# Optimization experiments

Hardware: AMD Instinct MI355X
Metric: run time of the kernel (lower is better)

The kernel has to match this reference:

```python
import jax, jax.numpy as jnp
import numpy as np
from jax import lax

V, E, H = 10000, 512, 512
B, L, T = 128, 8, 48


def setup_inputs() -> dict:
    key = jax.random.key(0)
    ks = jax.random.split(key, 12)
    s = lambda k, shape: jax.random.normal(k, shape, jnp.float32) * 0.05
    kw_lens = jnp.sort(jax.random.randint(ks[2], (B,), 1, L + 1))[::-1]  # descending, as pack_padded requires
    return {
        "kws": jax.random.randint(ks[0], (B, L), 0, V),
        "poem": jax.random.randint(ks[1], (B, T), 0, V),
        "kw_lens": kw_lens,
        "embedding": s(ks[3], (V, E)),
        "enc_Wih": s(ks[4], (4 * H, E)), "enc_Whh": s(ks[5], (4 * H, H)), "enc_b": s(ks[6], (4 * H,)),
        "dec_Wih": s(ks[7], (4 * H, E)), "dec_Whh": s(ks[8], (4 * H, H)), "dec_b": s(ks[9], (4 * H,)),
        "out_W": s(ks[10], (V, 2 * H)), "out_b": s(ks[11], (V,)),
    }


def _lstm_step(h, c, x, Wih, Whh, b):
    # PyTorch gate order: i, f, g, o
    gates = x @ Wih.T + h @ Whh.T + b  # [B, 4H]
    i, f, g, o = jnp.split(gates, 4, axis=-1)
    c = jax.nn.sigmoid(f) * c + jax.nn.sigmoid(i) * jnp.tanh(g)
    h = jax.nn.sigmoid(o) * jnp.tanh(c)
    return h, c


def reference(kws, poem, kw_lens, embedding, enc_Wih, enc_Whh, enc_b,
              dec_Wih, dec_Whh, dec_b, out_W, out_b):
    bs = kws.shape[0]
    mask = jnp.arange(L)[None, :] < kw_lens[:, None]  # sequence_mask, [B, L]

    # ---- encoder LSTM over keywords (dropout inactive at eval) ----
    kws_emb = embedding[kws]  # [B, L, E]

    def enc_scan(carry, x):
        h, c = carry
        h, c = _lstm_step(h, c, x, enc_Wih, enc_Whh, enc_b)
        return (h, c), (h, c)

    z = jnp.zeros((bs, H), embedding.dtype)
    _, (hs, cs) = lax.scan(enc_scan, (z, z), kws_emb.transpose(1, 0, 2))  # [L, B, H]
    kws_rep = hs.transpose(1, 0, 2) * mask[..., None]  # pad_packed zeros past length
    # pack semantics: final hidden is the state at the last valid timestep
    bidx = jnp.arange(bs)
    h0 = hs[kw_lens - 1, bidx]
    c0 = cs[kw_lens - 1, bidx]

    # ---- greedy per-timestep decode with dot-product attention ----
    neg = jnp.asarray(-1e9, embedding.dtype)

    def dec_scan(carry, tok):
        h, c = carry
        x = embedding[tok]  # [B, E]
        h, c = _lstm_step(h, c, x, dec_Wih, dec_Whh, dec_b)
        scores = jnp.einsum('bh,blh->bl', h, kws_rep)
        attn = jax.nn.softmax(jnp.where(mask, scores, neg), axis=-1)
        ctx = jnp.einsum('bl,blh->bh', attn, kws_rep)
        logits = jnp.concatenate([h, ctx], axis=-1) @ out_W.T + out_b  # [B, V]
        return (h, c), logits

    _, preds = lax.scan(dec_scan, (h0, c0), poem.T)  # [T, B, V]
    return preds.transpose(1, 0, 2)  # [B, T, V]
```

## Files before the change

kernel.cpp:

```cpp
#include <hip/hip_runtime.h>
#include <hip/hip_bf16.h>

typedef __bf16 bf16;
typedef __attribute__((ext_vector_type(8))) __bf16 bf16x8;
typedef __attribute__((ext_vector_type(4))) __bf16 bf16x4;
typedef __attribute__((ext_vector_type(4))) float f32x4;

#define B_ 128
#define L_ 8
#define T_ 48
#define V_ 10000
#define NBLK_REC 32

__device__ __forceinline__ float sigf(float x) { return 1.f / (1.f + expf(-x)); }

__device__ __forceinline__ void gl_lds16(const bf16* g, bf16* l) {
  __builtin_amdgcn_global_load_lds(
      (const __attribute__((address_space(1))) unsigned int*)g,
      (__attribute__((address_space(3))) unsigned int*)l, 16, 0, 0);
}

__device__ __forceinline__ unsigned aload32(const void* p) {
  return __hip_atomic_load((unsigned*)p, __ATOMIC_RELAXED, __HIP_MEMORY_SCOPE_AGENT);
}
__device__ __forceinline__ void astore64(void* p, unsigned long long v) {
  __hip_atomic_store((unsigned long long*)p, v, __ATOMIC_RELAXED, __HIP_MEMORY_SCOPE_AGENT);
}
__device__ __forceinline__ float bflo(unsigned u) { return __uint_as_float(u << 16); }
__device__ __forceinline__ float bfhi(unsigned u) { return __uint_as_float(u & 0xffff0000u); }
__device__ __forceinline__ unsigned packbf(float lo, float hi) {
  bf16 a = (bf16)lo, b = (bf16)hi;
  unsigned short ua = __builtin_bit_cast(unsigned short, a);
  unsigned short ub = __builtin_bit_cast(unsigned short, b);
  return (unsigned)ua | ((unsigned)ub << 16);
}

__device__ __forceinline__ void signal(unsigned* flg, int blk, unsigned step) {
  asm volatile("s_waitcnt vmcnt(0)" ::: "memory");
  __syncthreads();
  if (threadIdx.x == 0)
    __hip_atomic_store(flg + blk * 32, step, __ATOMIC_RELAXED, __HIP_MEMORY_SCOPE_AGENT);
}
__device__ __forceinline__ void waitstep(const unsigned* flg, unsigned step) {
  if (threadIdx.x < 64) {
    int lane = threadIdx.x;
    for (;;) {
      unsigned v = (lane < NBLK_REC) ? aload32(flg + lane * 32) : step;
      if (__all((int)(v >= step))) break;
      __builtin_amdgcn_s_sleep(1);
    }
  }
  __syncthreads();
}

__global__ void prep_kernel(
    const int* __restrict__ kws, const int* __restrict__ poem,
    const float* __restrict__ emb,
    const float* __restrict__ eWih, const float* __restrict__ eWhh,
    const float* __restrict__ dWih, const float* __restrict__ dWhh,
    const float* __restrict__ outW,
    bf16* __restrict__ WihE, bf16* __restrict__ WhhE,
    bf16* __restrict__ WihD, bf16* __restrict__ WhhD,
    bf16* __restrict__ outWb,
    bf16* __restrict__ Xenc, bf16* __restrict__ Xdec,
    unsigned* __restrict__ flg)
{
  if (blockIdx.x == 0)
    for (int i = threadIdx.x; i < 1024; i += blockDim.x) flg[i] = 0u;
  const long SW = 1048576;
  const long SOWP = 10354688;
  const long SXE = 524288;
  const long SXD = 3145728;
  const long total = 4 * SW + SOWP + SXE + SXD;
  for (long i = blockIdx.x * (long)blockDim.x + threadIdx.x; i < total;
       i += (long)gridDim.x * blockDim.x) {
    long j = i;
    if (j < SW) { WihE[j] = (bf16)eWih[j]; continue; } j -= SW;
    if (j < SW) { WhhE[j] = (bf16)eWhh[j]; continue; } j -= SW;
    if (j < SW) { WihD[j] = (bf16)dWih[j]; continue; } j -= SW;
    if (j < SW) { WhhD[j] = (bf16)dWhh[j]; continue; } j -= SW;
    if (j < SOWP) {
      long r = j >> 10;
      outWb[j] = (r < 10000) ? (bf16)outW[j] : (bf16)0.f;
      continue;
    } j -= SOWP;
    if (j < SXE) {
      int e = (int)(j & 511); int b = (int)((j >> 9) & 127); int l = (int)(j >> 16);
      int tok = kws[b * L_ + l];
      Xenc[j] = (bf16)emb[(long)tok * 512 + e];
      continue;
    } j -= SXE;
    {
      int e = (int)(j & 511); int b = (int)((j >> 9) & 127); int t = (int)(j >> 16);
      int tok = poem[b * T_ + t];
      Xdec[j] = (bf16)emb[(long)tok * 512 + e];
    }
  }
}

template<int MODE>
__global__ __launch_bounds__(256) void gemm2_kernel(
    const bf16* __restrict__ A, const bf16* __restrict__ Bm,
    const float* __restrict__ bias, void* __restrict__ outp,
    int M, int N, int K, int MT)
{
  __shared__ bf16 As[128 * 32];
  __shared__ bf16 Bs[128 * 32];
  const int tid = threadIdx.x, lane = tid & 63, wid = tid >> 6;
  const int nwg = gridDim.x;
  int bid = blockIdx.x;
  int tm, tn;
  if (MODE == 2) {
    int xcd = bid & 7, idx = bid >> 3;
    tm = xcd * 6 + idx % 6;
    tn = idx / 6;
  } else {
    int swz = ((nwg & 7) == 0) ? ((bid & 7) * (nwg >> 3) + (bid >> 3)) : bid;
    tm = swz % MT; tn = swz / MT;
  }
  const int m0 = tm * 128, n0 = tn * 128;
  const int wm = (wid >> 1) * 64, wn = (wid & 1) * 64;
  const int fr = lane & 15, ku = lane >> 4;

  f32x4 acc[4][4];
  #pragma unroll
  for (int mi = 0; mi < 4; ++mi)
    #pragma unroll
    for (int ni = 0; ni < 4; ++ni) {
      acc[mi][ni][0] = 0.f; acc[mi][ni][1] = 0.f;
      acc[mi][ni][2] = 0.f; acc[mi][ni][3] = 0.f;
    }

  for (int kt = 0; kt < K; kt += 32) {
    #pragma unroll
    for (int j = 0; j < 2; ++j) {
      int i0 = j * 256 + wid * 64;
      int i = i0 + lane;
      int r = i >> 2, ub = i & 3;
      gl_lds16(A + (size_t)(m0 + r) * K + kt + ub * 8, As + (size_t)i0 * 8);
      gl_lds16(Bm + (size_t)(n0 + r) * K + kt + ub * 8, Bs + (size_t)i0 * 8);
    }
    __syncthreads();
    bf16x8 af[4], bfr[4];
    #pragma unroll
    for (int mi = 0; mi < 4; ++mi)
      af[mi] = *(const bf16x8*)(As + (size_t)(wm + mi * 16 + fr) * 32 + ku * 8);
    #pragma unroll
    for (int ni = 0; ni < 4; ++ni)
      bfr[ni] = *(const bf16x8*)(Bs + (size_t)(wn + ni * 16 + fr) * 32 + ku * 8);
    #pragma unroll
    for (int mi = 0; mi < 4; ++mi)
      #pragma unroll
      for (int ni = 0; ni < 4; ++ni)
        acc[mi][ni] = __builtin_amdgcn_mfma_f32_16x16x32_bf16(af[mi], bfr[ni], acc[mi][ni], 0, 0, 0);
    __syncthreads();
  }

  const int fq = (lane >> 4) * 4;
  #pragma unroll
  for (int mi = 0; mi < 4; ++mi) {
    #pragma unroll
    for (int ni = 0; ni < 4; ++ni) {
      #pragma unroll
      for (int j = 0; j < 4; ++j) {
        int r = m0 + wm + mi * 16 + fq + j;
        int cix = n0 + wn + ni * 16 + fr;
        if (cix < N) {
          float v = acc[mi][ni][j] + bias[cix];
          if (MODE == 2) {
            int b = r & 127, t = r >> 7;
            ((float*)outp)[(size_t)b * (T_ * V_) + (size_t)t * V_ + cix] = v;
          } else {
            ((bf16*)outp)[((size_t)(r >> 7) * 2048 + cix) * 128 + (r & 127)] = (bf16)v;
          }
        }
      }
    }
  }
}

__global__ __launch_bounds__(256, 1) void recurrent_kernel(
    const bf16* __restrict__ preEncT, const bf16* __restrict__ preDecT,
    const bf16* __restrict__ WhhE, const bf16* __restrict__ WhhD,
    const int* __restrict__ kwl,
    bf16* __restrict__ hS,
    bf16* __restrict__ h0b,
    bf16* __restrict__ hsEnc,
    bf16* __restrict__ Hcat,
    unsigned* __restrict__ flg)
{
  __shared__ bf16 Bs[64 * 512];
  __shared__ bf16 As[128 * 256];
  const int tid = threadIdx.x, lane = tid & 63, wid = tid >> 6;
  const int blk = blockIdx.x, n0 = blk * 16;
  const int fr = lane & 15, fq = (lane >> 4) * 4, ku = lane >> 4;
  const int axor = fr & 7;
  const int arow0 = wid * 32 + fr, arow1 = wid * 32 + 16 + fr;
  const int row0 = wid * 32 + fq, row1 = wid * 32 + 16 + fq;
  const int brow = tid >> 1, bhalf = tid & 1;
  const int blen = kwl[brow];
  const int batt = blk * 4 + wid;
  const int lenb = kwl[batt];
  int lenr[2][4];
  #pragma unroll
  for (int j = 0; j < 4; ++j) { lenr[0][j] = kwl[row0 + j]; lenr[1][j] = kwl[row1 + j]; }

  auto loadB = [&](const bf16* W) {
    #pragma unroll
    for (int j = 0; j < 16; ++j) {
      int i = j * 256 + tid;
      int r = i >> 6, u = i & 63;
      int p = u ^ (r & 7);
      bf16x8 v = *(const bf16x8*)(W + (size_t)((r >> 4) * 512 + n0 + (r & 15)) * 512 + u * 8);
      *(bf16x8*)(Bs + (size_t)r * 512 + p * 8) = v;
    }
  };

  f32x4 acc[2][4];
  auto zacc = [&]() {
    #pragma unroll
    for (int mi = 0; mi < 2; ++mi)
      #pragma unroll
      for (int g = 0; g < 4; ++g) {
        acc[mi][g][0] = 0.f; acc[mi][g][1] = 0.f;
        acc[mi][g][2] = 0.f; acc[mi][g][3] = 0.f;
      }
  };

  auto gemm_full = [&](const bf16* h_in) {
    #pragma unroll
    for (int ch = 0; ch < 2; ++ch) {
      f32x4 tv[16];
      #pragma unroll
      for (int j = 0; j < 16; ++j) {
        int i = j * 256 + tid;
        int r = i >> 5, up = i & 31;
        const bf16* ga = h_in + (size_t)r * 512 + ch * 256 + up * 8;
        asm volatile("global_load_dwordx4 %0, %1, off sc0 sc1"
                     : "=v"(tv[j]) : "v"(ga) : "memory");
      }
      asm volatile("s_waitcnt vmcnt(0)" ::: "memory");
      __builtin_amdgcn_sched_barrier(0);
      #pragma unroll
      for (int j = 0; j < 16; ++j) {
        int i = j * 256 + tid;
        int r = i >> 5, up = i & 31;
        int s = up ^ (r & 7);
        *(f32x4*)(As + ((size_t)r * 32 + s) * 8) = tv[j];
      }
      __syncthreads();
      #pragma unroll
      for (int kt = 0; kt < 8; ++kt) {
        int cA = (kt * 4 + ku) ^ axor;
        int cB = ((ch * 8 + kt) * 4 + ku) ^ axor;
        bf16x8 af0 = *(const bf16x8*)(As + (size_t)arow0 * 256 + cA * 8);
        bf16x8 af1 = *(const bf16x8*)(As + (size_t)arow1 * 256 + cA * 8);
        #pragma unroll
        for (int g = 0; g < 4; ++g) {
          bf16x8 bv = *(const bf16x8*)(Bs + (size_t)(g * 16 + fr) * 512 + cB * 8);
          acc[0][g] = __builtin_amdgcn_mfma_f32_16x16x32_bf16(af0, bv, acc[0][g], 0, 0, 0);
          acc[1][g] = __builtin_amdgcn_mfma_f32_16x16x32_bf16(af1, bv, acc[1][g], 0, 0, 0);
        }
      }
      __syncthreads();
    }
  };

  float cr[2][4] = {{0.f,0.f,0.f,0.f},{0.f,0.f,0.f,0.f}};
  float c0r[2][4] = {{0.f,0.f,0.f,0.f},{0.f,0.f,0.f,0.f}};
  bf16 hout[2][4];

  bf16x4 gv[2][4];
  auto prefg = [&](const bf16* preT) {
    #pragma unroll
    for (int mi = 0; mi < 2; ++mi) {
      int rbase = mi ? row1 : row0;
      int hcol = n0 + fr;
      #pragma unroll
      for (int g = 0; g < 4; ++g)
        gv[mi][g] = *(const bf16x4*)(preT + ((size_t)(g * 512 + hcol)) * 128 + rbase);
    }
  };

  auto pointwise = [&]() {
    #pragma unroll
    for (int mi = 0; mi < 2; ++mi) {
      #pragma unroll
      for (int j = 0; j < 4; ++j) {
        float gi = acc[mi][0][j] + (float)gv[mi][0][j];
        float gf = acc[mi][1][j] + (float)gv[mi][1][j];
        float gg = acc[mi][2][j] + (float)gv[mi][2][j];
        float go = acc[mi][3][j] + (float)gv[mi][3][j];
        float cn = sigf(gf) * cr[mi][j] + sigf(gi) * tanhf(gg);
        float hn = sigf(go) * tanhf(cn);
        cr[mi][j] = cn;
        hout[mi][j] = (bf16)hn;
      }
    }
  };

  auto bounce_store = [&](bf16* hdst, bf16* hsdst, int t, int is_enc) {
    #pragma unroll
    for (int mi = 0; mi < 2; ++mi) {
      int rbase = mi ? row1 : row0;
      #pragma unroll
      for (int j = 0; j < 4; ++j)
        As[(size_t)(rbase + j) * 16 + fr] = hout[mi][j];
    }
    __syncthreads();
    unsigned long long v0 = *(unsigned long long*)(As + (size_t)brow * 16 + bhalf * 8);
    unsigned long long v1 = *(unsigned long long*)(As + (size_t)brow * 16 + bhalf * 8 + 4);
    size_t off = (size_t)brow * 512 + n0 + bhalf * 8;
    astore64(hdst + off, v0);
    astore64(hdst + off + 4, v1);
    if (is_enc) {
      unsigned long long m0 = (t < blen) ? v0 : 0ull;
      unsigned long long m1 = (t < blen) ? v1 : 0ull;
      astore64(hsdst + off, m0);
      astore64(hsdst + off + 4, m1);
      if (t == blen - 1) {
        astore64(h0b + off, v0);
        astore64(h0b + off + 4, v1);
      }
    }
  };

  unsigned hatt[4];
  auto load_hatt = [&](const bf16* h_in) {
    #pragma unroll
    for (int e = 0; e < 4; ++e)
      hatt[e] = aload32(h_in + (size_t)batt * 512 + lane * 2 + 128 * e);
  };

  unsigned hsr[8][4];

  auto attention = [&](int tprev) {
    float sc[8];
    #pragma unroll
    for (int l = 0; l < 8; ++l) {
      float p = 0.f;
      #pragma unroll
      for (int e = 0; e < 4; ++e)
        p += bflo(hatt[e]) * bflo(hsr[l][e]) + bfhi(hatt[e]) * bfhi(hsr[l][e]);
      #pragma unroll
      for (int off = 32; off; off >>= 1) p += __shfl_xor(p, off);
      sc[l] = p;
    }
    float m = -1e30f;
    #pragma unroll
    for (int l = 0; l < 8; ++l) m = fmaxf(m, (l < lenb) ? sc[l] : -1e30f);
    float wgt[8]; float den = 0.f;
    #pragma unroll
    for (int l = 0; l < 8; ++l) { wgt[l] = (l < lenb) ? expf(sc[l] - m) : 0.f; den += wgt[l]; }
    float inv = 1.f / den;
    bf16* dst = Hcat + ((size_t)tprev * 128 + batt) * 1024;
    #pragma unroll
    for (int e = 0; e < 4; ++e) {
      float clo = 0.f, chi = 0.f;
      #pragma unroll
      for (int l = 0; l < 8; ++l) {
        clo += wgt[l] * bflo(hsr[l][e]);
        chi += wgt[l] * bfhi(hsr[l][e]);
      }
      *(unsigned*)(dst + 512 + lane * 2 + 128 * e) = packbf(clo * inv, chi * inv);
      *(unsigned*)(dst + lane * 2 + 128 * e) = hatt[e];
    }
  };

  loadB(WhhE);
  __syncthreads();
  for (int t = 0; t < 8; ++t) {
    prefg(preEncT + (size_t)t * 262144);
    zacc();
    if (t > 0) {
      waitstep(flg, (unsigned)t);
      gemm_full(hS + (size_t)(t - 1) * 65536);
    }
    pointwise();
    #pragma unroll
    for (int mi = 0; mi < 2; ++mi)
      #pragma unroll
      for (int j = 0; j < 4; ++j)
        if (t == lenr[mi][j] - 1) c0r[mi][j] = cr[mi][j];
    bounce_store(hS + (size_t)t * 65536, hsEnc + (size_t)t * 65536, t, 1);
    signal(flg, blk, (unsigned)(t + 1));
  }

  __syncthreads();
  loadB(WhhD);
  __syncthreads();
  waitstep(flg, 8u);
  #pragma unroll
  for (int l = 0; l < 8; ++l)
    #pragma unroll
    for (int e = 0; e < 4; ++e)
      hsr[l][e] = aload32(hsEnc + ((size_t)l * 128 + batt) * 512 + lane * 2 + 128 * e);
  #pragma unroll
  for (int mi = 0; mi < 2; ++mi)
    #pragma unroll
    for (int j = 0; j < 4; ++j) cr[mi][j] = c0r[mi][j];

  for (int t = 0; t < 48; ++t) {
    prefg(preDecT + (size_t)t * 262144);
    zacc();
    const bf16* hin = (t == 0) ? (const bf16*)h0b : (const bf16*)(hS + (size_t)(8 + t - 1) * 65536);
    waitstep(flg, (unsigned)(8 + t));
    gemm_full(hin);
    pointwise();
    bounce_store(hS + (size_t)(8 + t) * 65536, nullptr, t, 0);
    signal(flg, blk, (unsigned)(9 + t));
    if (t >= 1) {
      load_hatt(hin);
      attention(t - 1);
    }
  }
  waitstep(flg, 56u);
  load_hatt(hS + (size_t)55 * 65536);
  attention(47);
}

extern "C" void kernel_launch(void* const* d_in, const int* in_sizes, int n_in,
                              void* d_out, int out_size, void* d_ws, size_t ws_size,
                              hipStream_t stream)
{
  const int* kws  = (const int*)d_in[0];
  const int* poem = (const int*)d_in[1];
  const int* kwl  = (const int*)d_in[2];
  const float* emb  = (const float*)d_in[3];
  const float* eWih = (const float*)d_in[4];
  const float* eWhh = (const float*)d_in[5];
  const float* eb   = (const float*)d_in[6];
  const float* dWih = (const float*)d_in[7];
  const float* dWhh = (const float*)d_in[8];
  const float* db   = (const float*)d_in[9];
  const float* outW = (const float*)d_in[10];
  const float* outb = (const float*)d_in[11];
  float* out = (float*)d_out;

  char* base = (char*)d_ws;
  size_t o = 0;
  auto take = [&](size_t bytes) -> char* {
    char* r = base + o;
    o += (bytes + 255) & ~(size_t)255;
    return r;
  };
  bf16* WihE  = (bf16*)take(2048 * 512 * 2);
  bf16* WhhE  = (bf16*)take(2048 * 512 * 2);
  bf16* WihD  = (bf16*)take(2048 * 512 * 2);
  bf16* WhhD  = (bf16*)take(2048 * 512 * 2);
  bf16* outWb = (bf16*)take((size_t)10112 * 1024 * 2);
  bf16* Xenc  = (bf16*)take(1024 * 512 * 2);
  bf16* Xdec  = (bf16*)take((size_t)6144 * 512 * 2);
  bf16* preEncT = (bf16*)take((size_t)8 * 2048 * 128 * 2);
  bf16* preDecT = (bf16*)take((size_t)48 * 2048 * 128 * 2);
  bf16* Hcat   = (bf16*)take((size_t)6144 * 1024 * 2);
  bf16* hS     = (bf16*)take((size_t)56 * 65536 * 2);
  bf16* hsEnc  = (bf16*)take((size_t)8 * 128 * 512 * 2);
  bf16* h0b    = (bf16*)take(128 * 512 * 2);
  unsigned* flg = (unsigned*)take(4096);

  prep_kernel<<<4096, 256, 0, stream>>>(kws, poem, emb, eWih, eWhh, dWih, dWhh, outW,
                                        WihE, WhhE, WihD, WhhD, outWb, Xenc, Xdec, flg);

  gemm2_kernel<3><<<128, 256, 0, stream>>>(Xenc, WihE, eb, preEncT, 1024, 2048, 512, 8);
  gemm2_kernel<3><<<768, 256, 0, stream>>>(Xdec, WihD, db, preDecT, 6144, 2048, 512, 48);

  recurrent_kernel<<<NBLK_REC, 256, 0, stream>>>(preEncT, preDecT, WhhE, WhhD, kwl,
                                                 hS, h0b, hsEnc, Hcat, flg);

  gemm2_kernel<2><<<3792, 256, 0, stream>>>(Hcat, outWb, outb, out, 6144, 10000, 1024, 48);
}
```

Measured before the change: 788.1 us.

## Confine recurrent LSTM to 16 blocks on one XCD with gate-interleaved layout

The recurrent kernel now launches 128 blocks, and each block reads its XCC_ID and claims a role through atomics. Only the first 16 blocks on the first XCD to fill up keep running, so the per-step flag barrier and h exchange stay within one XCD's L2 and can use sc0 loads and stores instead of device-scope coherent traffic. Each block holds a 128x512 slice of Whh in LDS covering all four gates interleaved, and the pre-activation layout is changed to put the gates adjacent, so the pointwise step reads gates locally. Risks include wasted blocks, a timeout-based fallback if the XCD election fails, and a heavier per-block GEMM.

```diff
diff --git a/kernel.cpp b/kernel.cpp
--- a/kernel.cpp
+++ b/kernel.cpp
@@ -10,7 +10,8 @@
 #define L_ 8
 #define T_ 48
 #define V_ 10000
-#define NBLK_REC 32
+#define NB 128
+#define ROLES 16
 
 __device__ __forceinline__ float sigf(float x) { return 1.f / (1.f + expf(-x)); }
 
@@ -19,12 +20,15 @@
       (const __attribute__((address_space(1))) unsigned int*)g,
       (__attribute__((address_space(3))) unsigned int*)l, 16, 0, 0);
 }
-
-__device__ __forceinline__ unsigned aload32(const void* p) {
-  return __hip_atomic_load((unsigned*)p, __ATOMIC_RELAXED, __HIP_MEMORY_SCOPE_AGENT);
-}
-__device__ __forceinline__ void astore64(void* p, unsigned long long v) {
-  __hip_atomic_store((unsigned long long*)p, v, __ATOMIC_RELAXED, __HIP_MEMORY_SCOPE_AGENT);
+__device__ __forceinline__ void gl_lds16_c(const bf16* g, bf16* l) {
+  __builtin_amdgcn_global_load_lds(
+      (const __attribute__((address_space(1))) unsigned int*)g,
+      (__attribute__((address_space(3))) unsigned int*)l, 16, 0, 1);
+}
+
+__device__ __forceinline__ void st2_sc0(bf16* p, unsigned short v) {
+  unsigned v32 = v;
+  asm volatile("global_store_short %0, %1, off sc0" :: "v"(p), "v"(v32) : "memory");
 }
 __device__ __forceinline__ float bflo(unsigned u) { return __uint_as_float(u << 16); }
 __device__ __forceinline__ float bfhi(unsigned u) { return __uint_as_float(u & 0xffff0000u); }
@@ -33,24 +37,6 @@
   unsigned short ua = __builtin_bit_cast(unsigned short, a);
   unsigned short ub = __builtin_bit_cast(unsigned short, b);
   return (unsigned)ua | ((unsigned)ub << 16);
-}
-
-__device__ __forceinline__ void signal(unsigned* flg, int blk, unsigned step) {
-  asm volatile("s_waitcnt vmcnt(0)" ::: "memory");
-  __syncthreads();
-  if (threadIdx.x == 0)
-    __hip_atomic_store(flg + blk * 32, step, __ATOMIC_RELAXED, __HIP_MEMORY_SCOPE_AGENT);
-}
-__device__ __forceinline__ void waitstep(const unsigned* flg, unsigned step) {
-  if (threadIdx.x < 64) {
-    int lane = threadIdx.x;
-    for (;;) {
-      unsigned v = (lane < NBLK_REC) ? aload32(flg + lane * 32) : step;
-      if (__all((int)(v >= step))) break;
-      __builtin_amdgcn_s_sleep(1);
-    }
-  }
-  __syncthreads();
 }
 
 __global__ void prep_kernel(
@@ -63,10 +49,10 @@
     bf16* __restrict__ WihD, bf16* __restrict__ WhhD,
     bf16* __restrict__ outWb,
     bf16* __restrict__ Xenc, bf16* __restrict__ Xdec,
-    unsigned* __restrict__ flg)
+    unsigned* __restrict__ ctl)
 {
   if (blockIdx.x == 0)
-    for (int i = threadIdx.x; i < 1024; i += blockDim.x) flg[i] = 0u;
+    for (int i = threadIdx.x; i < 8192; i += blockDim.x) ctl[i] = 0u;
   const long SW = 1048576;
   const long SOWP = 10354688;
   const long SXE = 524288;
@@ -171,7 +157,9 @@
             int b = r & 127, t = r >> 7;
             ((float*)outp)[(size_t)b * (T_ * V_) + (size_t)t * V_ + cix] = v;
           } else {
-            ((bf16*)outp)[((size_t)(r >> 7) * 2048 + cix) * 128 + (r & 127)] = (bf16)v;
+            int t = r >> 7, b = r & 127;
+            int hcol = cix & 511, g = cix >> 9;
+            ((bf16*)outp)[(((size_t)t * 512 + hcol) * 128 + b) * 4 + g] = (bf16)v;
           }
         }
       }
@@ -183,238 +171,272 @@
     const bf16* __restrict__ preEncT, const bf16* __restrict__ preDecT,
     const bf16* __restrict__ WhhE, const bf16* __restrict__ WhhD,
     const int* __restrict__ kwl,
-    bf16* __restrict__ hS,
-    bf16* __restrict__ h0b,
-    bf16* __restrict__ hsEnc,
-    bf16* __restrict__ Hcat,
-    unsigned* __restrict__ flg)
+    bf16* __restrict__ hS, bf16* __restrict__ h0b,
+    bf16* __restrict__ hsEnc, bf16* __restrict__ Hcat,
+    unsigned* __restrict__ ctl)
 {
-  __shared__ bf16 Bs[64 * 512];
-  __shared__ bf16 As[128 * 256];
+  __shared__ bf16 Wlds[128 * 512];
+  __shared__ bf16 Hb[128 * 128];
+  int* s_info = (int*)Hb;
   const int tid = threadIdx.x, lane = tid & 63, wid = tid >> 6;
-  const int blk = blockIdx.x, n0 = blk * 16;
-  const int fr = lane & 15, fq = (lane >> 4) * 4, ku = lane >> 4;
-  const int axor = fr & 7;
-  const int arow0 = wid * 32 + fr, arow1 = wid * 32 + 16 + fr;
-  const int row0 = wid * 32 + fq, row1 = wid * 32 + 16 + fq;
-  const int brow = tid >> 1, bhalf = tid & 1;
-  const int blen = kwl[brow];
-  const int batt = blk * 4 + wid;
-  const int lenb = kwl[batt];
-  int lenr[2][4];
+
+  if (tid == 0) {
+    unsigned xcd;
+    asm volatile("s_getreg_b32 %0, hwreg(HW_REG_XCC_ID)" : "=s"(xcd));
+    xcd &= 7u;
+    unsigned r = __hip_atomic_fetch_add(ctl + xcd, 1u, __ATOMIC_RELAXED, __HIP_MEMORY_SCOPE_AGENT);
+    asm volatile("s_waitcnt vmcnt(0)" ::: "memory");
+    __hip_atomic_fetch_add(ctl + 8, 1u, __ATOMIC_RELAXED, __HIP_MEMORY_SCOPE_AGENT);
+    int iters = 0;
+    while (__hip_atomic_load(ctl + 8, __ATOMIC_RELAXED, __HIP_MEMORY_SCOPE_AGENT) < NB &&
+           iters++ < (1 << 20))
+      __builtin_amdgcn_s_sleep(8);
+    int win = -1;
+    for (int x = 0; x < 8; ++x) {
+      unsigned c = __hip_atomic_load(ctl + x, __ATOMIC_RELAXED, __HIP_MEMORY_SCOPE_AGENT);
+      if (win < 0 && c >= ROLES) win = x;
+    }
+    s_info[0] = (int)r;
+    s_info[1] = ((int)xcd == win && r < ROLES) ? 1 : 0;
+    s_info[2] = (int)xcd;
+  }
+  __syncthreads();
+  const int role = s_info[0];
+  const int ok = s_info[1];
+  const int myxcd = s_info[2];
+  __syncthreads();
+  if (!ok) return;
+  unsigned* flgx = ctl + 512 + myxcd * (ROLES * 32);
+  unsigned* myflag = flgx + role * 32;
+
+  const int fr = lane & 15, ku = lane >> 4;
+  const int wm2 = wid >> 1, wn2 = wid & 1;
+  const int b0 = (role * 4 + wid) * 2;
+  const int lenb0 = kwl[b0], lenb1 = kwl[b0 + 1];
+  int lenB[4];
   #pragma unroll
-  for (int j = 0; j < 4; ++j) { lenr[0][j] = kwl[row0 + j]; lenr[1][j] = kwl[row1 + j]; }
-
-  auto loadB = [&](const bf16* W) {
-    #pragma unroll
-    for (int j = 0; j < 16; ++j) {
-      int i = j * 256 + tid;
+  for (int ni = 0; ni < 4; ++ni) lenB[ni] = kwl[wn2 * 64 + ni * 16 + fr];
+
+  auto signal = [&](unsigned step) {
+    asm volatile("s_waitcnt vmcnt(0)" ::: "memory");
+    __syncthreads();
+    if (tid == 0)
+      asm volatile("global_store_dword %0, %1, off sc0" :: "v"(myflag), "v"(step) : "memory");
+  };
+  auto waitstep = [&](unsigned step) {
+    if (tid < 64) {
+      const unsigned* fp = flgx + (tid & 15) * 32;
+      const bool act = tid < ROLES;
+      int iters = 0;
+      for (;;) {
+        unsigned v = step;
+        if (act)
+          asm volatile("global_load_dword %0, %1, off sc0\n\ts_waitcnt vmcnt(0)"
+                       : "=v"(v) : "v"(fp) : "memory");
+        if (__all((int)(v >= step)) || iters++ > (1 << 20)) break;
+        __builtin_amdgcn_s_sleep(2);
+      }
+    }
+    __syncthreads();
+  };
+
+  auto loadW = [&](const bf16* W) {
+    #pragma unroll
+    for (int q = 0; q < 32; ++q) {
+      int i = q * 256 + tid;
       int r = i >> 6, u = i & 63;
-      int p = u ^ (r & 7);
-      bf16x8 v = *(const bf16x8*)(W + (size_t)((r >> 4) * 512 + n0 + (r & 15)) * 512 + u * 8);
-      *(bf16x8*)(Bs + (size_t)r * 512 + p * 8) = v;
-    }
-  };
-
-  f32x4 acc[2][4];
+      int j5 = r >> 2, g = r & 3;
+      bf16x8 v = *(const bf16x8*)(W + (size_t)(g * 512 + role * 32 + j5) * 512 + u * 8);
+      *(bf16x8*)(Wlds + ((size_t)r * 64 + (u ^ (r & 15))) * 8) = v;
+    }
+  };
+
+  f32x4 acc[4][4];
   auto zacc = [&]() {
     #pragma unroll
-    for (int mi = 0; mi < 2; ++mi)
-      #pragma unroll
-      for (int g = 0; g < 4; ++g) {
-        acc[mi][g][0] = 0.f; acc[mi][g][1] = 0.f;
-        acc[mi][g][2] = 0.f; acc[mi][g][3] = 0.f;
-      }
-  };
-
-  auto gemm_full = [&](const bf16* h_in) {
-    #pragma unroll
-    for (int ch = 0; ch < 2; ++ch) {
-      f32x4 tv[16];
-      #pragma unroll
-      for (int j = 0; j < 16; ++j) {
-        int i = j * 256 + tid;
-        int r = i >> 5, up = i & 31;
-        const bf16* ga = h_in + (size_t)r * 512 + ch * 256 + up * 8;
-        asm volatile("global_load_dwordx4 %0, %1, off sc0 sc1"
-                     : "=v"(tv[j]) : "v"(ga) : "memory");
-      }
-      asm volatile("s_waitcnt vmcnt(0)" ::: "memory");
-      __builtin_amdgcn_sched_barrier(0);
-      #pragma unroll
-      for (int j = 0; j < 16; ++j) {
-        int i = j * 256 + tid;
-        int r = i >> 5, up = i & 31;
-        int s = up ^ (r & 7);
-        *(f32x4*)(As + ((size_t)r * 32 + s) * 8) = tv[j];
+    for (int mi = 0; mi < 4; ++mi)
+      #pragma unroll
+      for (int ni = 0; ni < 4; ++ni) {
+        acc[mi][ni][0] = 0.f; acc[mi][ni][1] = 0.f;
+        acc[mi][ni][2] = 0.f; acc[mi][ni][3] = 0.f;
+      }
+  };
+
+  auto do_gemm = [&](const bf16* hbuf) {
+    #pragma unroll
+    for (int ch = 0; ch < 4; ++ch) {
+      #pragma unroll
+      for (int q = 0; q < 8; ++q) {
+        int i0 = q * 256 + wid * 64;
+        int i = i0 + lane;
+        int row = i >> 4, u = i & 15;
+        gl_lds16_c(hbuf + (size_t)row * 512 + ch * 128 + ((u ^ (row & 15)) * 8),
+                   Hb + (size_t)i0 * 8);
       }
       __syncthreads();
       #pragma unroll
-      for (int kt = 0; kt < 8; ++kt) {
-        int cA = (kt * 4 + ku) ^ axor;
-        int cB = ((ch * 8 + kt) * 4 + ku) ^ axor;
-        bf16x8 af0 = *(const bf16x8*)(As + (size_t)arow0 * 256 + cA * 8);
-        bf16x8 af1 = *(const bf16x8*)(As + (size_t)arow1 * 256 + cA * 8);
-        #pragma unroll
-        for (int g = 0; g < 4; ++g) {
-          bf16x8 bv = *(const bf16x8*)(Bs + (size_t)(g * 16 + fr) * 512 + cB * 8);
-          acc[0][g] = __builtin_amdgcn_mfma_f32_16x16x32_bf16(af0, bv, acc[0][g], 0, 0, 0);
-          acc[1][g] = __builtin_amdgcn_mfma_f32_16x16x32_bf16(af1, bv, acc[1][g], 0, 0, 0);
+      for (int kt = 0; kt < 4; ++kt) {
+        bf16x8 af[4], bfv[4];
+        #pragma unroll
+        for (int mi = 0; mi < 4; ++mi) {
+          int r = wm2 * 64 + mi * 16 + fr;
+          int uk = (ch * 4 + kt) * 4 + ku;
+          af[mi] = *(const bf16x8*)(Wlds + ((size_t)r * 64 + (uk ^ (r & 15))) * 8);
         }
+        #pragma unroll
+        for (int ni = 0; ni < 4; ++ni) {
+          int row = wn2 * 64 + ni * 16 + fr;
+          int uk = kt * 4 + ku;
+          bfv[ni] = *(const bf16x8*)(Hb + ((size_t)row * 16 + (uk ^ (row & 15))) * 8);
+        }
+        #pragma unroll
+        for (int mi = 0; mi < 4; ++mi)
+          #pragma unroll
+          for (int ni = 0; ni < 4; ++ni)
+            acc[mi][ni] = __builtin_amdgcn_mfma_f32_16x16x32_bf16(af[mi], bfv[ni], acc[mi][ni], 0, 0, 0);
       }
       __syncthreads();
     }
   };
 
-  float cr[2][4] = {{0.f,0.f,0.f,0.f},{0.f,0.f,0.f,0.f}};
-  float c0r[2][4] = {{0.f,0.f,0.f,0.f},{0.f,0.f,0.f,0.f}};
-  bf16 hout[2][4];
-
-  bf16x4 gv[2][4];
+  float cst[4][4] = {}, c0[4][4] = {};
+  bf16x4 gv[4][4];
   auto prefg = [&](const bf16* preT) {
     #pragma unroll
-    for (int mi = 0; mi < 2; ++mi) {
-      int rbase = mi ? row1 : row0;
-      int hcol = n0 + fr;
-      #pragma unroll
-      for (int g = 0; g < 4; ++g)
-        gv[mi][g] = *(const bf16x4*)(preT + ((size_t)(g * 512 + hcol)) * 128 + rbase);
-    }
-  };
-
-  auto pointwise = [&]() {
-    #pragma unroll
-    for (int mi = 0; mi < 2; ++mi) {
-      #pragma unroll
-      for (int j = 0; j < 4; ++j) {
-        float gi = acc[mi][0][j] + (float)gv[mi][0][j];
-        float gf = acc[mi][1][j] + (float)gv[mi][1][j];
-        float gg = acc[mi][2][j] + (float)gv[mi][2][j];
-        float go = acc[mi][3][j] + (float)gv[mi][3][j];
-        float cn = sigf(gf) * cr[mi][j] + sigf(gi) * tanhf(gg);
+    for (int mi = 0; mi < 4; ++mi) {
+      int hcol = role * 32 + wm2 * 16 + mi * 4 + ku;
+      #pragma unroll
+      for (int ni = 0; ni < 4; ++ni) {
+        int batch = wn2 * 64 + ni * 16 + fr;
+        gv[mi][ni] = *(const bf16x4*)(preT + (((size_t)hcol * 128) + batch) * 4);
+      }
+    }
+  };
+
+  auto pointwise = [&](int t, bf16* hdst, int is_enc, bf16* hsdst) {
+    #pragma unroll
+    for (int mi = 0; mi < 4; ++mi) {
+      const int hcol = role * 32 + wm2 * 16 + mi * 4 + ku;
+      #pragma unroll
+      for (int ni = 0; ni < 4; ++ni) {
+        const int batch = wn2 * 64 + ni * 16 + fr;
+        float gi = acc[mi][ni][0] + (float)gv[mi][ni][0];
+        float gf = acc[mi][ni][1] + (float)gv[mi][ni][1];
+        float gg = acc[mi][ni][2] + (float)gv[mi][ni][2];
+        float go = acc[mi][ni][3] + (float)gv[mi][ni][3];
+        float cn = sigf(gf) * cst[mi][ni] + sigf(gi) * tanhf(gg);
         float hn = sigf(go) * tanhf(cn);
-        cr[mi][j] = cn;
-        hout[mi][j] = (bf16)hn;
-      }
-    }
-  };
-
-  auto bounce_store = [&](bf16* hdst, bf16* hsdst, int t, int is_enc) {
-    #pragma unroll
-    for (int mi = 0; mi < 2; ++mi) {
-      int rbase = mi ? row1 : row0;
-      #pragma unroll
-      for (int j = 0; j < 4; ++j)
-        As[(size_t)(rbase + j) * 16 + fr] = hout[mi][j];
-    }
-    __syncthreads();
-    unsigned long long v0 = *(unsigned long long*)(As + (size_t)brow * 16 + bhalf * 8);
-    unsigned long long v1 = *(unsigned long long*)(As + (size_t)brow * 16 + bhalf * 8 + 4);
-    size_t off = (size_t)brow * 512 + n0 + bhalf * 8;
-    astore64(hdst + off, v0);
-    astore64(hdst + off + 4, v1);
-    if (is_enc) {
-      unsigned long long m0 = (t < blen) ? v0 : 0ull;
-      unsigned long long m1 = (t < blen) ? v1 : 0ull;
-      astore64(hsdst + off, m0);
-      astore64(hsdst + off + 4, m1);
-      if (t == blen - 1) {
-        astore64(h0b + off, v0);
-        astore64(h0b + off + 4, v1);
-      }
-    }
-  };
-
-  unsigned hatt[4];
+        cst[mi][ni] = cn;
+        unsigned short hb = __builtin_bit_cast(unsigned short, (bf16)hn);
+        st2_sc0(hdst + (size_t)batch * 512 + hcol, hb);
+        if (is_enc) {
+          int len = lenB[ni];
+          st2_sc0(hsdst + (size_t)batch * 512 + hcol, (t < len) ? hb : (unsigned short)0);
+          if (t == len - 1) {
+            st2_sc0(h0b + (size_t)batch * 512 + hcol, hb);
+            c0[mi][ni] = cn;
+          }
+        }
+      }
+    }
+  };
+
+  unsigned hatt[2][4], hsr[2][8][4];
   auto load_hatt = [&](const bf16* h_in) {
     #pragma unroll
-    for (int e = 0; e < 4; ++e)
-      hatt[e] = aload32(h_in + (size_t)batt * 512 + lane * 2 + 128 * e);
-  };
-
-  unsigned hsr[8][4];
-
+    for (int bb = 0; bb < 2; ++bb)
+      #pragma unroll
+      for (int e = 0; e < 4; ++e) {
+        const bf16* p = h_in + (size_t)(b0 + bb) * 512 + lane * 2 + 128 * e;
+        asm volatile("global_load_dword %0, %1, off sc0" : "=v"(hatt[bb][e]) : "v"(p) : "memory");
+      }
+  };
   auto attention = [&](int tprev) {
-    float sc[8];
-    #pragma unroll
-    for (int l = 0; l < 8; ++l) {
-      float p = 0.f;
-      #pragma unroll
-      for (int e = 0; e < 4; ++e)
-        p += bflo(hatt[e]) * bflo(hsr[l][e]) + bfhi(hatt[e]) * bfhi(hsr[l][e]);
-      #pragma unroll
-      for (int off = 32; off; off >>= 1) p += __shfl_xor(p, off);
-      sc[l] = p;
-    }
-    float m = -1e30f;
-    #pragma unroll
-    for (int l = 0; l < 8; ++l) m = fmaxf(m, (l < lenb) ? sc[l] : -1e30f);
-    float wgt[8]; float den = 0.f;
-    #pragma unroll
-    for (int l = 0; l < 8; ++l) { wgt[l] = (l < lenb) ? expf(sc[l] - m) : 0.f; den += wgt[l]; }
-    float inv = 1.f / den;
-    bf16* dst = Hcat + ((size_t)tprev * 128 + batt) * 1024;
-    #pragma unroll
-    for (int e = 0; e < 4; ++e) {
-      float clo = 0.f, chi = 0.f;
+    asm volatile("s_waitcnt vmcnt(0)" ::: "memory");
+    __builtin_amdgcn_sched_barrier(0);
+    #pragma unroll
+    for (int bb = 0; bb < 2; ++bb) {
+      const int b = b0 + bb;
+      const int len = bb ? lenb1 : lenb0;
+      float sc[8];
       #pragma unroll
       for (int l = 0; l < 8; ++l) {
-        clo += wgt[l] * bflo(hsr[l][e]);
-        chi += wgt[l] * bfhi(hsr[l][e]);
-      }
-      *(unsigned*)(dst + 512 + lane * 2 + 128 * e) = packbf(clo * inv, chi * inv);
-      *(unsigned*)(dst + lane * 2 + 128 * e) = hatt[e];
-    }
-  };
-
-  loadB(WhhE);
+        float p = 0.f;
+        #pragma unroll
+        for (int e = 0; e < 4; ++e)
+          p += bflo(hatt[bb][e]) * bflo(hsr[bb][l][e]) + bfhi(hatt[bb][e]) * bfhi(hsr[bb][l][e]);
+        #pragma unroll
+        for (int off = 32; off; off >>= 1) p += __shfl_xor(p, off);
+        sc[l] = p;
+      }
+      float m = -1e30f;
+      #pragma unroll
+      for (int l = 0; l < 8; ++l) m = fmaxf(m, (l < len) ? sc[l] : -1e30f);
+      float wgt[8]; float den = 0.f;
+      #pragma unroll
+      for (int l = 0; l < 8; ++l) { wgt[l] = (l < len) ? expf(sc[l] - m) : 0.f; den += wgt[l]; }
+      float inv = 1.f / den;
+      bf16* dst = Hcat + ((size_t)tprev * 128 + b) * 1024;
+      #pragma unroll
+      for (int e = 0; e < 4; ++e) {
+        float clo = 0.f, chi = 0.f;
+        #pragma unroll
+        for (int l = 0; l < 8; ++l) {
+          clo += wgt[l] * bflo(hsr[bb][l][e]);
+          chi += wgt[l] * bfhi(hsr[bb][l][e]);
+        }
+        *(unsigned*)(dst + 512 + lane * 2 + 128 * e) = packbf(clo * inv, chi * inv);
+        *(unsigned*)(dst + lane * 2 + 128 * e) = hatt[bb][e];
+      }
+    }
+  };
+
+  loadW(WhhE);
   __syncthreads();
   for (int t = 0; t < 8; ++t) {
     prefg(preEncT + (size_t)t * 262144);
     zacc();
     if (t > 0) {
-      waitstep(flg, (unsigned)t);
-      gemm_full(hS + (size_t)(t - 1) * 65536);
-    }
-    pointwise();
-    #pragma unroll
-    for (int mi = 0; mi < 2; ++mi)
-      #pragma unroll
-      for (int j = 0; j < 4; ++j)
-        if (t == lenr[mi][j] - 1) c0r[mi][j] = cr[mi][j];
-    bounce_store(hS + (size_t)t * 65536, hsEnc + (size_t)t * 65536, t, 1);
-    signal(flg, blk, (unsigned)(t + 1));
+      waitstep((unsigned)t);
+      do_gemm(hS + (size_t)(t - 1) * 65536);
+    }
+    pointwise(t, hS + (size_t)t * 65536, 1, hsEnc + (size_t)t * 65536);
+    signal((unsigned)(t + 1));
   }
 
   __syncthreads();
-  loadB(WhhD);
+  loadW(WhhD);
   __syncthreads();
-  waitstep(flg, 8u);
+  waitstep(8u);
   #pragma unroll
-  for (int l = 0; l < 8; ++l)
-    #pragma unroll
-    for (int e = 0; e < 4; ++e)
-      hsr[l][e] = aload32(hsEnc + ((size_t)l * 128 + batt) * 512 + lane * 2 + 128 * e);
+  for (int bb = 0; bb < 2; ++bb)
+    #pragma unroll
+    for (int l = 0; l < 8; ++l)
+      #pragma unroll
+      for (int e = 0; e < 4; ++e) {
+        const bf16* p = hsEnc + (size_t)l * 65536 + (size_t)(b0 + bb) * 512 + lane * 2 + 128 * e;
+        asm volatile("global_load_dword %0, %1, off sc0" : "=v"(hsr[bb][l][e]) : "v"(p) : "memory");
+      }
+  asm volatile("s_waitcnt vmcnt(0)" ::: "memory");
+  __builtin_amdgcn_sched_barrier(0);
   #pragma unroll
-  for (int mi = 0; mi < 2; ++mi)
-    #pragma unroll
-    for (int j = 0; j < 4; ++j) cr[mi][j] = c0r[mi][j];
+  for (int mi = 0; mi < 4; ++mi)
+    #pragma unroll
+    for (int ni = 0; ni < 4; ++ni) cst[mi][ni] = c0[mi][ni];
 
   for (int t = 0; t < 48; ++t) {
     prefg(preDecT + (size_t)t * 262144);
     zacc();
-    const bf16* hin = (t == 0) ? (const bf16*)h0b : (const bf16*)(hS + (size_t)(8 + t - 1) * 65536);
-    waitstep(flg, (unsigned)(8 + t));
-    gemm_full(hin);
-    pointwise();
-    bounce_store(hS + (size_t)(8 + t) * 65536, nullptr, t, 0);
-    signal(flg, blk, (unsigned)(9 + t));
-    if (t >= 1) {
-      load_hatt(hin);
-      attention(t - 1);
-    }
-  }
-  waitstep(flg, 56u);
+    const bf16* hin = (t == 0) ? (const bf16*)h0b
+                               : (const bf16*)(hS + (size_t)(8 + t - 1) * 65536);
+    waitstep((unsigned)(8 + t));
+    load_hatt(hin);
+    do_gemm(hin);
+    pointwise(t, hS + (size_t)(8 + t) * 65536, 0, nullptr);
+    signal((unsigned)(9 + t));
+    if (t >= 1) attention(t - 1);
+  }
+  waitstep(56u);
   load_hatt(hS + (size_t)55 * 65536);
   attention(47);
 }
@@ -457,16 +479,16 @@
   bf16* hS     = (bf16*)take((size_t)56 * 65536 * 2);
   bf16* hsEnc  = (bf16*)take((size_t)8 * 128 * 512 * 2);
   bf16* h0b    = (bf16*)take(128 * 512 * 2);
-  unsigned* flg = (unsigned*)take(4096);
+  unsigned* ctl = (unsigned*)take(32768);
 
   prep_kernel<<<4096, 256, 0, stream>>>(kws, poem, emb, eWih, eWhh, dWih, dWhh, outW,
-                                        WihE, WhhE, WihD, WhhD, outWb, Xenc, Xdec, flg);
+                                        WihE, WhhE, WihD, WhhD, outWb, Xenc, Xdec, ctl);
 
   gemm2_kernel<3><<<128, 256, 0, stream>>>(Xenc, WihE, eb, preEncT, 1024, 2048, 512, 8);
   gemm2_kernel<3><<<768, 256, 0, stream>>>(Xdec, WihD, db, preDecT, 6144, 2048, 512, 48);
 
-  recurrent_kernel<<<NBLK_REC, 256, 0, stream>>>(preEncT, preDecT, WhhE, WhhD, kwl,
-                                                 hS, h0b, hsEnc, Hcat, flg);
+  recurrent_kernel<<<NB, 256, 0, stream>>>(preEncT, preDecT, WhhE, WhhD, kwl,
+                                           hS, h0b, hsEnc, Hcat, ctl);
 
   gemm2_kernel<2><<<3792, 256, 0, stream>>>(Hcat, outWb, outb, out, 6144, 10000, 1024, 48);
 }
```

Measured after the change: 1.251 ms. 58.8% more time.
